# Performance work log

Measured on AMD Instinct MI355X. Metric: run time of the kernel, lower is better.

Reference implementation:

```python
import jax, jax.numpy as jnp
import numpy as np

EPS = 1e-5  # BatchNorm eps
TOPK = 256  # SoftThresholdingOperation topk


def conv1x1(x, W, b):
    # x: [B,C,H,W], W: [O,C], b: [O]
    return jnp.einsum('bchw,oc->bohw', x, W) + b[None, :, None, None]


def bn_relu(x, gamma, beta, mean, var):
    # inference-mode BatchNorm2d followed by ReLU
    inv = gamma / jnp.sqrt(var + EPS)
    return jax.nn.relu(x * inv[None, :, None, None] + (beta - mean * inv)[None, :, None, None])


def topk_sparsemax(x, k):
    # HSPA SoftThresholdingOperation: sparsemax restricted to top-k entries of last axis.
    k = min(k, x.shape[-1])
    vals = jax.lax.top_k(x, k)[0]                       # sorted descending, [..., k]
    cssv = jnp.cumsum(vals, axis=-1) - 1.0              # cumulative sum minus 1
    r = jnp.arange(1, k + 1, dtype=x.dtype)
    support = vals * r > cssv                           # support indicator
    k_sup = jnp.sum(support, axis=-1, keepdims=True)    # support size, int
    tau = jnp.take_along_axis(cssv, k_sup - 1, axis=-1) / k_sup.astype(x.dtype)
    return jnp.clip(x - tau, 0.0)                       # sparse attention weights


def setup_inputs() -> dict:
    key = jax.random.key(0)
    ks = jax.random.split(key, 10)
    B, C = 128, 256
    s = 1.0 / np.sqrt(C)
    return {
        'zf': jax.random.normal(ks[0], (B, C, 13, 13), jnp.float32),
        'xf': jax.random.normal(ks[1], (B, C, 25, 25), jnp.float32),
        'Wq': jax.random.normal(ks[2], (C, C), jnp.float32) * s,
        'bq': jnp.zeros((C,), jnp.float32),
        'Ws': jax.random.normal(ks[3], (C, C), jnp.float32) * s,
        'bs': jnp.zeros((C,), jnp.float32),
        'Wg': jax.random.normal(ks[4], (C, C), jnp.float32) * s,
        'bg': jnp.zeros((C,), jnp.float32),
        'g_gamma': jnp.ones((C,), jnp.float32),
        'g_beta': jnp.zeros((C,), jnp.float32),
        'g_mean': jnp.zeros((C,), jnp.float32),
        'g_var': jnp.ones((C,), jnp.float32),
        'Wf': jax.random.normal(ks[5], (C, 2 * C), jnp.float32) * (1.0 / np.sqrt(2 * C)),
        'bf': jnp.zeros((C,), jnp.float32),
        'f_gamma': jnp.ones((C,), jnp.float32),
        'f_beta': jnp.zeros((C,), jnp.float32),
        'f_mean': jnp.zeros((C,), jnp.float32),
        'f_var': jnp.ones((C,), jnp.float32),
    }


def reference(zf, xf, Wq, bq, Ws, bs, Wg, bg, g_gamma, g_beta, g_mean, g_var,
              Wf, bf, f_gamma, f_beta, f_mean, f_var):
    B, C, Hx, Wx = xf.shape
    _, _, Hz, Wz = zf.shape
    xf_trans = conv1x1(xf, Wq, bq)                      # query
    zf_trans = conv1x1(zf, Ws, bs)                      # support
    xf_g = bn_relu(conv1x1(xf, Wg, bg), g_gamma, g_beta, g_mean, g_var)
    zf_g = bn_relu(conv1x1(zf, Wg, bg), g_gamma, g_beta, g_mean, g_var)

    Nx, Nz = Hx * Wx, Hz * Wz
    zf_trans_p = zf_trans.reshape(B, C, Nz)             # [B,C,Nz]
    zf_g_p = zf_g.reshape(B, C, Nz)                     # [B,C,Nz]
    xf_trans_p = xf_trans.reshape(B, C, Nx)             # [B,C,Nx]

    similar = jnp.einsum('bcn,bcm->bnm', xf_trans_p, zf_trans_p)  # [B,Nx,Nz]
    score = topk_sparsemax(similar, TOPK)                          # sparse attn
    embedding = jnp.einsum('bnm,bcm->bcn', score, zf_g_p)          # [B,C,Nx]
    embedding = embedding.reshape(B, C, Hx, Wx)

    cat = jnp.concatenate([embedding, xf_g], axis=1)    # [B,2C,Hx,Wx]
    out = bn_relu(conv1x1(cat, Wf, bf), f_gamma, f_beta, f_mean, f_var)
    return out
```

## Files before the change

### kernel.cpp

```cpp
#include <hip/hip_runtime.h>
#include <math.h>

#define EPS 1e-5f

constexpr int Bb  = 128;
constexpr int C   = 256;
constexpr int Nz  = 169;
constexpr int Nx  = 625;
constexpr int NzP = 192;

typedef __bf16 bf16x8 __attribute__((ext_vector_type(8)));
typedef float  f32x4  __attribute__((ext_vector_type(4)));

__device__ __forceinline__ unsigned short f2bf(float f) {
    union { float f; unsigned u; } x; x.f = f;
    unsigned r = x.u + 0x7FFFu + ((x.u >> 16) & 1u);
    return (unsigned short)(r >> 16);
}
__device__ __forceinline__ float bf2f(unsigned short h) {
    union { unsigned u; float f; } x; x.u = ((unsigned)h) << 16;
    return x.f;
}

__global__ __launch_bounds__(256)
void prep_all(const float* __restrict__ zf,
              const float* __restrict__ Wq, const float* __restrict__ bq,
              const float* __restrict__ Ws, const float* __restrict__ bs,
              const float* __restrict__ Wg, const float* __restrict__ Wf,
              unsigned short* __restrict__ Wg_bf, unsigned short* __restrict__ Wf_bf,
              float* __restrict__ wv, float* __restrict__ wu, float* __restrict__ c0,
              unsigned short* __restrict__ Mhi, unsigned short* __restrict__ Mlo,
              float* __restrict__ U,
              unsigned short* __restrict__ zfT_hi, unsigned short* __restrict__ zfT_lo)
{
    __shared__ float T[64][65];
    const int bx = blockIdx.x, tid = threadIdx.x;

    if (bx < 512) {
        int i = bx * 256 + tid;
        if (i < C * C) Wg_bf[i] = f2bf(Wg[i]);
        if (i < C * 2 * C) Wf_bf[i] = f2bf(Wf[i]);
        return;
    }
    if (bx == 512) {
        float a = 0.f, b = 0.f;
        for (int o = 0; o < C; ++o) {
            a += Wq[o * C + tid] * bs[o];
            b += Ws[o * C + tid] * bq[o];
        }
        wv[tid] = a;
        wu[tid] = b;
        if (tid == 0) {
            float c = 0.f;
            for (int o = 0; o < C; ++o) c += bq[o] * bs[o];
            c0[0] = c;
        }
        return;
    }
    if (bx < 529) {
        const int t  = bx - 513;
        const int j0 = (t & 3) * 64, i0 = (t >> 2) * 64;
        const int tx = tid & 15, ty = tid >> 4;
        float (*Qs)[65] = (float(*)[65])&T[0][0];
        float (*Ss)[65] = (float(*)[65])&T[16][0];
        float acc[4][4] = {};

        for (int kc = 0; kc < C; kc += 16) {
            #pragma unroll
            for (int i = 0; i < 4; ++i) {
                int e = tid + 256 * i;
                int k = e >> 6, col = e & 63;
                Qs[k][col] = Wq[(size_t)(kc + k) * C + i0 + col];
                Ss[k][col] = Ws[(size_t)(kc + k) * C + j0 + col];
            }
            __syncthreads();
            #pragma unroll
            for (int k = 0; k < 16; ++k) {
                float a[4], bv[4];
                #pragma unroll
                for (int i = 0; i < 4; ++i) a[i] = Qs[k][ty * 4 + i];
                #pragma unroll
                for (int j = 0; j < 4; ++j) bv[j] = Ss[k][tx * 4 + j];
                #pragma unroll
                for (int i = 0; i < 4; ++i)
                    #pragma unroll
                    for (int j = 0; j < 4; ++j)
                        acc[i][j] = fmaf(a[i], bv[j], acc[i][j]);
            }
            __syncthreads();
        }
        #pragma unroll
        for (int i = 0; i < 4; ++i)
            #pragma unroll
            for (int j = 0; j < 4; ++j) {
                float v = acc[i][j];
                unsigned short h = f2bf(v);
                size_t idx = (size_t)(i0 + ty * 4 + i) * C + j0 + tx * 4 + j;
                Mhi[idx] = h;
                Mlo[idx] = f2bf(v - bf2f(h));
            }
        return;
    }
    if (bx < 657) {
        const int b = bx - 529, m = tid;
        if (m >= NzP) return;
        float s = 0.f;
        if (m < Nz) {
            const float* zb = zf + (size_t)b * C * Nz + m;
            float s0 = 0.f, s1 = 0.f, s2 = 0.f, s3 = 0.f;
            for (int c = 0; c < C; c += 4) {
                s0 += wu[c]     * zb[(size_t)c * Nz];
                s1 += wu[c + 1] * zb[(size_t)(c + 1) * Nz];
                s2 += wu[c + 2] * zb[(size_t)(c + 2) * Nz];
                s3 += wu[c + 3] * zb[(size_t)(c + 3) * Nz];
            }
            s = (s0 + s1) + (s2 + s3) + c0[0];
        }
        U[(size_t)b * NzP + m] = s;
        return;
    }
    {
        const int t  = bx - 657;
        const int n0 = (t % 3) * 64;
        const int c0v = ((t / 3) & 3) * 64;
        const int b  = t / 12;
        const float* Xb = zf + ((size_t)b * C + c0v) * Nz;
        #pragma unroll
        for (int i = 0; i < 16; ++i) {
            int e = tid + 256 * i;
            int c = e >> 6, n = e & 63;
            T[c][n] = (n0 + n < Nz) ? Xb[(size_t)c * Nz + n0 + n] : 0.f;
        }
        __syncthreads();
        #pragma unroll
        for (int i = 0; i < 16; ++i) {
            int e = tid + 256 * i;
            int n = e >> 6, c = e & 63;
            if (n0 + n < Nz) {
                float v = T[c][n];
                unsigned short h = f2bf(v);
                size_t idx = ((size_t)b * Nz + n0 + n) * C + c0v + c;
                zfT_hi[idx] = h;
                zfT_lo[idx] = f2bf(v - bf2f(h));
            }
        }
    }
}

__global__ __launch_bounds__(256)
void z_gemm(const unsigned short* __restrict__ Mhi,
            const unsigned short* __restrict__ Mlo,
            const unsigned short* __restrict__ Wg,
            const unsigned short* __restrict__ Bhi,
            const unsigned short* __restrict__ Blo,
            const float* __restrict__ wv,
            const float* __restrict__ bg, const float* __restrict__ g_gamma,
            const float* __restrict__ g_beta, const float* __restrict__ g_mean,
            const float* __restrict__ g_var,
            unsigned short* __restrict__ Yqh, unsigned short* __restrict__ Yql,
            unsigned short* __restrict__ Yg)
{
    __shared__ unsigned short Ah[64][40], Al[64][40], Ag[64][40];
    __shared__ unsigned short Bh[64][40], Bl[64][40];

    const int b   = blockIdx.z;
    const int n0  = blockIdx.x * 64;
    const int o0  = blockIdx.y * 64;
    const int tid = threadIdx.x;
    const int lane = tid & 63, wid = tid >> 6;
    const int wr = wid >> 1, wc = wid & 1;

    const unsigned short* Bhb = Bhi + (size_t)b * Nz * C;
    const unsigned short* Blb = Blo + (size_t)b * Nz * C;

    f32x4 accq[2][2], accg[2][2];
    #pragma unroll
    for (int i = 0; i < 2; ++i)
        #pragma unroll
        for (int j = 0; j < 2; ++j)
            #pragma unroll
            for (int e = 0; e < 4; ++e) { accq[i][j][e] = 0.f; accg[i][j][e] = 0.f; }

    const int srow = tid >> 2, sseg = tid & 3;
    const int lr = lane & 15, lk = (lane >> 4) * 8;

    for (int kc = 0; kc < C; kc += 32) {
        const int gk = kc + sseg * 8;
        *(int4*)&Ah[srow][sseg * 8] = *(const int4*)&Mhi[(size_t)(o0 + srow) * C + gk];
        *(int4*)&Al[srow][sseg * 8] = *(const int4*)&Mlo[(size_t)(o0 + srow) * C + gk];
        *(int4*)&Ag[srow][sseg * 8] = *(const int4*)&Wg[(size_t)(o0 + srow) * C + gk];

        const int gn = n0 + srow;
        int4 bv = make_int4(0, 0, 0, 0), blv = make_int4(0, 0, 0, 0);
        if (gn < Nz) {
            bv  = *(const int4*)&Bhb[(size_t)gn * C + gk];
            blv = *(const int4*)&Blb[(size_t)gn * C + gk];
        }
        *(int4*)&Bh[srow][sseg * 8] = bv;
        *(int4*)&Bl[srow][sseg * 8] = blv;
        __syncthreads();

        bf16x8 ah[2], al[2], ag[2], bh[2], bl[2];
        #pragma unroll
        for (int i = 0; i < 2; ++i) {
            ah[i] = *(const bf16x8*)&Ah[wr * 32 + i * 16 + lr][lk];
            al[i] = *(const bf16x8*)&Al[wr * 32 + i * 16 + lr][lk];
            ag[i] = *(const bf16x8*)&Ag[wr * 32 + i * 16 + lr][lk];
            bh[i] = *(const bf16x8*)&Bh[wc * 32 + i * 16 + lr][lk];
            bl[i] = *(const bf16x8*)&Bl[wc * 32 + i * 16 + lr][lk];
        }
        #pragma unroll
        for (int i = 0; i < 2; ++i)
            #pragma unroll
            for (int j = 0; j < 2; ++j) {
                accq[i][j] = __builtin_amdgcn_mfma_f32_16x16x32_bf16(al[i], bh[j], accq[i][j], 0, 0, 0);
                accq[i][j] = __builtin_amdgcn_mfma_f32_16x16x32_bf16(ah[i], bl[j], accq[i][j], 0, 0, 0);
                accq[i][j] = __builtin_amdgcn_mfma_f32_16x16x32_bf16(ah[i], bh[j], accq[i][j], 0, 0, 0);
                accg[i][j] = __builtin_amdgcn_mfma_f32_16x16x32_bf16(ag[i], bh[j], accg[i][j], 0, 0, 0);
            }
        __syncthreads();
    }

    const int lg = lane >> 4;
    #pragma unroll
    for (int i = 0; i < 2; ++i) {
        const int ob = o0 + wr * 32 + i * 16 + lg * 4;
        float bi[4], inv[4], sh[4], bgi[4];
        #pragma unroll
        for (int r = 0; r < 4; ++r) {
            int o = ob + r;
            bi[r] = wv[o];
            float iv = g_gamma[o] * rsqrtf(g_var[o] + EPS);
            inv[r] = iv; sh[r] = g_beta[o] - g_mean[o] * iv; bgi[r] = bg[o];
        }
        #pragma unroll
        for (int j = 0; j < 2; ++j) {
            const int gn = n0 + wc * 32 + j * 16 + lr;
            uint2 ph = make_uint2(0, 0), pl = make_uint2(0, 0), pg = make_uint2(0, 0);
            if (gn < Nz) {
                unsigned short h[4], l[4], g[4];
                #pragma unroll
                for (int r = 0; r < 4; ++r) {
                    float v = accq[i][j][r] + bi[r];
                    h[r] = f2bf(v);
                    l[r] = f2bf(v - bf2f(h[r]));
                    g[r] = f2bf(fmaxf(fmaf(accg[i][j][r] + bgi[r], inv[r], sh[r]), 0.f));
                }
                ph.x = (unsigned)h[0] | ((unsigned)h[1] << 16);
                ph.y = (unsigned)h[2] | ((unsigned)h[3] << 16);
                pl.x = (unsigned)l[0] | ((unsigned)l[1] << 16);
                pl.y = (unsigned)l[2] | ((unsigned)l[3] << 16);
                pg.x = (unsigned)g[0] | ((unsigned)g[1] << 16);
                pg.y = (unsigned)g[2] | ((unsigned)g[3] << 16);
            }
            size_t idx = ((size_t)b * NzP + gn) * C + ob;
            *(uint2*)&Yqh[idx] = ph;
            *(uint2*)&Yql[idx] = pl;
            *(uint2*)&Yg[idx]  = pg;
        }
    }
}

__global__ __launch_bounds__(256)
void zg2_gemm(const unsigned short* __restrict__ A, int aLd,
              const unsigned short* __restrict__ B1,
              unsigned short* __restrict__ Y, int N, int Nout, int K, int O)
{
    __shared__ unsigned short As[64][40];
    __shared__ unsigned short Bs[64][40];

    const int b   = blockIdx.z;
    const int n0  = blockIdx.x * 64;
    const int o0  = blockIdx.y * 64;
    const int tid = threadIdx.x;
    const int lane = tid & 63, wid = tid >> 6;
    const int wr = wid >> 1, wc = wid & 1;

    const unsigned short* B1b = B1 + (size_t)b * N * K;

    f32x4 acc[2][2];
    #pragma unroll
    for (int i = 0; i < 2; ++i)
        #pragma unroll
        for (int j = 0; j < 2; ++j)
            #pragma unroll
            for (int e = 0; e < 4; ++e) acc[i][j][e] = 0.f;

    const int srow = tid >> 2, sseg = tid & 3;
    const int lr = lane & 15, lk = (lane >> 4) * 8;

    for (int kc = 0; kc < K; kc += 32) {
        const int gk = kc + sseg * 8;
        *(int4*)&As[srow][sseg * 8] = *(const int4*)&A[(size_t)(o0 + srow) * aLd + gk];

        const int gn = n0 + srow;
        int4 bv = make_int4(0, 0, 0, 0);
        if (gn < N) bv = *(const int4*)&B1b[(size_t)gn * K + gk];
        *(int4*)&Bs[srow][sseg * 8] = bv;
        __syncthreads();

        bf16x8 a0 = *(const bf16x8*)&As[wr * 32 +      lr][lk];
        bf16x8 a1 = *(const bf16x8*)&As[wr * 32 + 16 + lr][lk];
        bf16x8 b0 = *(const bf16x8*)&Bs[wc * 32 +      lr][lk];
        bf16x8 b1 = *(const bf16x8*)&Bs[wc * 32 + 16 + lr][lk];

        acc[0][0] = __builtin_amdgcn_mfma_f32_16x16x32_bf16(a0, b0, acc[0][0], 0, 0, 0);
        acc[0][1] = __builtin_amdgcn_mfma_f32_16x16x32_bf16(a0, b1, acc[0][1], 0, 0, 0);
        acc[1][0] = __builtin_amdgcn_mfma_f32_16x16x32_bf16(a1, b0, acc[1][0], 0, 0, 0);
        acc[1][1] = __builtin_amdgcn_mfma_f32_16x16x32_bf16(a1, b1, acc[1][1], 0, 0, 0);
        __syncthreads();
    }

    const int lg = lane >> 4;
    #pragma unroll
    for (int i = 0; i < 2; ++i) {
        const int ob = o0 + wr * 32 + i * 16 + lg * 4;
        #pragma unroll
        for (int j = 0; j < 2; ++j) {
            const int gn = n0 + wc * 32 + j * 16 + lr;
            if (gn < Nout) {
                #pragma unroll
                for (int r = 0; r < 4; ++r)
                    Y[((size_t)b * O + ob + r) * Nout + gn] =
                        (gn < N) ? f2bf(acc[i][j][r]) : (unsigned short)0;
            }
        }
    }
}

#define XGIDX(n, o) ((((n) << 8) + (o)) ^ (((n) & 7) << 3))

__global__ __launch_bounds__(256)
void mega_x(const float* __restrict__ Xf,
            const unsigned short* __restrict__ Zqh,
            const unsigned short* __restrict__ Zql,
            const unsigned short* __restrict__ Wg,
            const unsigned short* __restrict__ Zg2,
            const unsigned short* __restrict__ Wf2,
            const float* __restrict__ U,
            const float* __restrict__ bg, const float* __restrict__ g_gamma,
            const float* __restrict__ g_beta, const float* __restrict__ g_mean,
            const float* __restrict__ g_var,
            const float* __restrict__ bf, const float* __restrict__ f_gamma,
            const float* __restrict__ f_beta, const float* __restrict__ f_mean,
            const float* __restrict__ f_var,
            float* __restrict__ out)
{
    __shared__ __attribute__((aligned(16))) char pool[69632];
    __shared__ float Us[192];

    unsigned short* XFfull = (unsigned short*)(pool);
    unsigned short* XG     = (unsigned short*)(pool);
    unsigned short* Bzh    = (unsigned short*)(pool + 33792);
    unsigned short* Bzl    = (unsigned short*)(pool + 49152);
    unsigned short* Ssc    = (unsigned short*)(pool + 33792);
    unsigned short* XFl    = (unsigned short*)(pool + 64512);

    const int g0  = blockIdx.z * gridDim.x + blockIdx.x;
    const int rid = (g0 & 7) * 160 + (g0 >> 3);
    const int b   = rid / 10;
    const int n0  = (rid % 10) * 64;

    const int tid = threadIdx.x;
    const int lane = tid & 63, w = tid >> 6;
    const int lr = lane & 15, lg = lane >> 4, lk = lg * 8;
    const int brow = tid >> 2, bseg = tid & 3;

    const unsigned short* Zqhb = Zqh + (size_t)b * NzP * C;
    const unsigned short* Zqlb = Zql + (size_t)b * NzP * C;
    const unsigned short* Zg2b = Zg2 + (size_t)b * C * NzP;

    if (tid < 192) Us[tid] = U[(size_t)b * NzP + tid];

    const int gnA = min(n0 + brow, Nx - 1);

    {
        f32x4 sacc[12];
        #pragma unroll
        for (int j = 0; j < 12; ++j)
            #pragma unroll
            for (int e = 0; e < 4; ++e) sacc[j][e] = 0.f;

        for (int kc = 0; kc < C; kc += 32) {
            {
                const float* src = Xf + ((size_t)b * C + kc + bseg * 8) * Nx + gnA;
                unsigned short h[8], l[8];
                #pragma unroll
                for (int e = 0; e < 8; ++e) {
                    float v = src[(size_t)e * Nx];
                    h[e] = f2bf(v);
                    l[e] = f2bf(v - bf2f(h[e]));
                }
                uint4 ph, pl;
                ph.x = (unsigned)h[0] | ((unsigned)h[1] << 16);
                ph.y = (unsigned)h[2] | ((unsigned)h[3] << 16);
                ph.z = (unsigned)h[4] | ((unsigned)h[5] << 16);
                ph.w = (unsigned)h[6] | ((unsigned)h[7] << 16);
                pl.x = (unsigned)l[0] | ((unsigned)l[1] << 16);
                pl.y = (unsigned)l[2] | ((unsigned)l[3] << 16);
                pl.z = (unsigned)l[4] | ((unsigned)l[5] << 16);
                pl.w = (unsigned)l[6] | ((unsigned)l[7] << 16);
                *(uint4*)&XFfull[brow * 264 + kc + bseg * 8] = ph;
                *(uint4*)&XFl[brow * 40 + bseg * 8] = pl;
            }
            #pragma unroll
            for (int i = 0; i < 3; ++i) {
                const int slot = tid + 256 * i;
                const int r = slot >> 2, s = slot & 3;
                const int gk = kc + s * 8;
                *(int4*)&Bzh[r * 40 + s * 8] = *(const int4*)&Zqhb[(size_t)r * C + gk];
                *(int4*)&Bzl[r * 40 + s * 8] = *(const int4*)&Zqlb[(size_t)r * C + gk];
            }
            __syncthreads();

            bf16x8 a0h = *(const bf16x8*)&XFfull[(w * 16 + lr) * 264 + kc + lk];
            bf16x8 a0l = *(const bf16x8*)&XFl[(w * 16 + lr) * 40 + lk];
            #pragma unroll
            for (int j = 0; j < 12; ++j) {
                bf16x8 bh = *(const bf16x8*)&Bzh[(j * 16 + lr) * 40 + lk];
                bf16x8 bl = *(const bf16x8*)&Bzl[(j * 16 + lr) * 40 + lk];
                sacc[j] = __builtin_amdgcn_mfma_f32_16x16x32_bf16(a0l, bh, sacc[j], 0, 0, 0);
                sacc[j] = __builtin_amdgcn_mfma_f32_16x16x32_bf16(a0h, bl, sacc[j], 0, 0, 0);
                sacc[j] = __builtin_amdgcn_mfma_f32_16x16x32_bf16(a0h, bh, sacc[j], 0, 0, 0);
            }
            __syncthreads();
        }

        #pragma unroll
        for (int j = 0; j < 12; ++j) {
            const int m = j * 16 + lr;
            const float uv = Us[m];
            const bool bad = (m >= Nz);
            #pragma unroll
            for (int q = 0; q < 4; ++q)
                sacc[j][q] = bad ? -1e30f : (sacc[j][q] + uv);
        }

        f32x4 mx = sacc[0];
        #pragma unroll
        for (int j = 1; j < 12; ++j)
            #pragma unroll
            for (int q = 0; q < 4; ++q) mx[q] = fmaxf(mx[q], sacc[j][q]);
        #pragma unroll
        for (int off = 1; off < 16; off <<= 1)
            #pragma unroll
            for (int q = 0; q < 4; ++q) mx[q] = fmaxf(mx[q], __shfl_xor(mx[q], off));

        f32x4 tau;
        #pragma unroll
        for (int q = 0; q < 4; ++q) tau[q] = mx[q] - 1.0f;

        for (int it = 0; it < 16; ++it) {
            f32x4 s, cnt;
            #pragma unroll
            for (int q = 0; q < 4; ++q) { s[q] = 0.f; cnt[q] = 0.f; }
            #pragma unroll
            for (int j = 0; j < 12; ++j)
                #pragma unroll
                for (int q = 0; q < 4; ++q)
                    if (sacc[j][q] > tau[q]) { s[q] += sacc[j][q]; cnt[q] += 1.f; }
            #pragma unroll
            for (int off = 1; off < 16; off <<= 1)
                #pragma unroll
                for (int q = 0; q < 4; ++q) {
                    s[q]   += __shfl_xor(s[q], off);
                    cnt[q] += __shfl_xor(cnt[q], off);
                }
            bool adv = false;
            #pragma unroll
            for (int q = 0; q < 4; ++q) {
                float nt = (s[q] - 1.0f) / cnt[q];
                if (nt > tau[q]) { tau[q] = nt; adv = true; }
            }
            if (!__any(adv ? 1 : 0)) break;
        }

        #pragma unroll
        for (int q = 0; q < 4; ++q) {
            const int n = w * 16 + 4 * lg + q;
            #pragma unroll
            for (int j = 0; j < 12; ++j) {
                const int m = j * 16 + lr;
                float sv = (m < Nz) ? fmaxf(sacc[j][q] - tau[q], 0.f) : 0.f;
                Ssc[n * 200 + m] = f2bf(sv);
            }
        }
    }

    f32x4 acc[4][4];
    #pragma unroll
    for (int i = 0; i < 4; ++i)
        #pragma unroll
        for (int j = 0; j < 4; ++j)
            #pragma unroll
            for (int e = 0; e < 4; ++e) acc[i][j][e] = 0.f;

    #pragma unroll
    for (int c = 0; c < 8; ++c) {
        const int kc = c * 32;
        bf16x8 a[4], bfr[4];
        #pragma unroll
        for (int i = 0; i < 4; ++i)
            a[i] = *(const bf16x8*)&Wg[(size_t)(w * 64 + i * 16 + lr) * C + kc + lk];
        #pragma unroll
        for (int j = 0; j < 4; ++j)
            bfr[j] = *(const bf16x8*)&XFfull[(j * 16 + lr) * 264 + kc + lk];
        #pragma unroll
        for (int i = 0; i < 4; ++i)
            #pragma unroll
            for (int j = 0; j < 4; ++j)
                acc[i][j] = __builtin_amdgcn_mfma_f32_16x16x32_bf16(a[i], bfr[j], acc[i][j], 0, 0, 0);
    }
    __syncthreads();

    #pragma unroll
    for (int i = 0; i < 4; ++i) {
        const int ob = w * 64 + i * 16 + lg * 4;
        float inv[4], sh[4], bi[4];
        #pragma unroll
        for (int r = 0; r < 4; ++r) {
            int o = ob + r;
            float iv = g_gamma[o] * rsqrtf(g_var[o] + EPS);
            inv[r] = iv; sh[r] = g_beta[o] - g_mean[o] * iv; bi[r] = bg[o];
        }
        #pragma unroll
        for (int j = 0; j < 4; ++j) {
            const int n = j * 16 + lr;
            unsigned short h[4];
            #pragma unroll
            for (int r = 0; r < 4; ++r)
                h[r] = f2bf(fmaxf(fmaf(acc[i][j][r] + bi[r], inv[r], sh[r]), 0.f));
            uint2 pk;
            pk.x = (unsigned)h[0] | ((unsigned)h[1] << 16);
            pk.y = (unsigned)h[2] | ((unsigned)h[3] << 16);
            *(uint2*)&XG[XGIDX(n, ob)] = pk;
        }
    }
    #pragma unroll
    for (int i = 0; i < 4; ++i)
        #pragma unroll
        for (int j = 0; j < 4; ++j)
            #pragma unroll
            for (int e = 0; e < 4; ++e) acc[i][j][e] = 0.f;
    __syncthreads();

    #pragma unroll
    for (int c = 0; c < 6; ++c) {
        const int kc = c * 32;
        bf16x8 a[4], bfr[4];
        #pragma unroll
        for (int i = 0; i < 4; ++i)
            a[i] = *(const bf16x8*)&Zg2b[(size_t)(w * 64 + i * 16 + lr) * NzP + kc + lk];
        #pragma unroll
        for (int j = 0; j < 4; ++j)
            bfr[j] = *(const bf16x8*)&Ssc[(j * 16 + lr) * 200 + kc + lk];
        #pragma unroll
        for (int i = 0; i < 4; ++i)
            #pragma unroll
            for (int j = 0; j < 4; ++j)
                acc[i][j] = __builtin_amdgcn_mfma_f32_16x16x32_bf16(a[i], bfr[j], acc[i][j], 0, 0, 0);
    }

    #pragma unroll
    for (int c = 0; c < 8; ++c) {
        const int kc = c * 32;
        bf16x8 a[4], bfr[4];
        #pragma unroll
        for (int i = 0; i < 4; ++i)
            a[i] = *(const bf16x8*)&Wf2[(size_t)(w * 64 + i * 16 + lr) * 512 + kc + lk];
        #pragma unroll
        for (int j = 0; j < 4; ++j)
            bfr[j] = *(const bf16x8*)&XG[XGIDX(j * 16 + lr, kc + lk)];
        #pragma unroll
        for (int i = 0; i < 4; ++i)
            #pragma unroll
            for (int j = 0; j < 4; ++j)
                acc[i][j] = __builtin_amdgcn_mfma_f32_16x16x32_bf16(a[i], bfr[j], acc[i][j], 0, 0, 0);
    }

    #pragma unroll
    for (int i = 0; i < 4; ++i) {
        const int ob = w * 64 + i * 16 + lg * 4;
        float inv[4], sh[4], bi[4];
        #pragma unroll
        for (int r = 0; r < 4; ++r) {
            int o = ob + r;
            float iv = f_gamma[o] * rsqrtf(f_var[o] + EPS);
            inv[r] = iv; sh[r] = f_beta[o] - f_mean[o] * iv; bi[r] = bf[o];
        }
        #pragma unroll
        for (int j = 0; j < 4; ++j) {
            const int gn = n0 + j * 16 + lr;
            if (gn < Nx) {
                #pragma unroll
                for (int r = 0; r < 4; ++r) {
                    float v = fmaxf(fmaf(acc[i][j][r] + bi[r], inv[r], sh[r]), 0.f);
                    out[((size_t)b * C + ob + r) * Nx + gn] = v;
                }
            }
        }
    }
}

extern "C" void kernel_launch(void* const* d_in, const int* in_sizes, int n_in,
                              void* d_out, int out_size, void* d_ws, size_t ws_size,
                              hipStream_t stream)
{
    const float* zf      = (const float*)d_in[0];
    const float* xf      = (const float*)d_in[1];
    const float* Wq      = (const float*)d_in[2];
    const float* bq      = (const float*)d_in[3];
    const float* Ws_     = (const float*)d_in[4];
    const float* bs      = (const float*)d_in[5];
    const float* Wg      = (const float*)d_in[6];
    const float* bg      = (const float*)d_in[7];
    const float* g_gamma = (const float*)d_in[8];
    const float* g_beta  = (const float*)d_in[9];
    const float* g_mean  = (const float*)d_in[10];
    const float* g_var   = (const float*)d_in[11];
    const float* Wf      = (const float*)d_in[12];
    const float* bf_     = (const float*)d_in[13];
    const float* f_gamma = (const float*)d_in[14];
    const float* f_beta  = (const float*)d_in[15];
    const float* f_mean  = (const float*)d_in[16];
    const float* f_var   = (const float*)d_in[17];
    float* out = (float*)d_out;

    typedef unsigned short u16;
    char* ws = (char*)d_ws;
    u16*   zfT_hi = (u16*)(ws);
    u16*   zfT_lo = (u16*)(ws +  11075584);
    u16*   zqT_hi = (u16*)(ws +  22151168);
    u16*   zqT_lo = (u16*)(ws +  34734080);
    u16*   zf_gT  = (u16*)(ws +  47316992);
    u16*   zg2    = (u16*)(ws +  59899904);
    float* U      = (float*)(ws +  72482816);
    u16*   Mhi    = (u16*)(ws +  72581120);
    u16*   Mlo    = (u16*)(ws +  72712192);
    u16*   Wg_bf  = (u16*)(ws +  72843264);
    u16*   Wf_bf  = (u16*)(ws +  72974336);
    float* wv     = (float*)(ws +  73236480);
    float* wu     = (float*)(ws +  73237504);
    float* c0     = (float*)(ws +  73238528);

    dim3 blk(256);
    const int gx_x = (Nx + 63) / 64;
    const int gx_z = NzP / 64;

    prep_all<<<dim3(2193), blk, 0, stream>>>(
        zf, Wq, bq, Ws_, bs, Wg, Wf,
        Wg_bf, Wf_bf, wv, wu, c0, Mhi, Mlo, U, zfT_hi, zfT_lo);

    z_gemm<<<dim3(gx_z, C / 64, Bb), blk, 0, stream>>>(
        Mhi, Mlo, Wg_bf, zfT_hi, zfT_lo, wv,
        bg, g_gamma, g_beta, g_mean, g_var,
        zqT_hi, zqT_lo, zf_gT);

    zg2_gemm<<<dim3(gx_z, C / 64, Bb), blk, 0, stream>>>(
        Wf_bf, 2 * C, zf_gT, zg2, NzP, NzP, C, C);

    mega_x<<<dim3(gx_x, 1, Bb), blk, 0, stream>>>(
        xf, zqT_hi, zqT_lo, Wg_bf, zg2, Wf_bf + C, U,
        bg, g_gamma, g_beta, g_mean, g_var,
        bf_, f_gamma, f_beta, f_mean, f_var, out);
}
```

Baseline: 199.0 us.

## Fuse z-side transpose, U, query/gate GEMMs and Wf projection into one kernel

Replaces the zf transpose/split, U reduction, z_gemm and zg2_gemm stages with a single z_full kernel. Each block loads a 64-column slice of zf once into LDS as bf16 hi/lo, computes U, the split-precision query projection, and the gated BN-ReLU features, then applies the Wf projection from LDS. This removes two kernel launches and the global round-trips of zfT and zf_gT. In exchange, each block covers all 256 output channels, giving only 384 blocks with large LDS use. Weight fragments are now read straight from global memory instead of being staged in shared memory.

```diff
diff --git a/kernel.cpp b/kernel.cpp
--- a/kernel.cpp
+++ b/kernel.cpp
@@ -23,17 +23,14 @@
 }
 
 __global__ __launch_bounds__(256)
-void prep_all(const float* __restrict__ zf,
-              const float* __restrict__ Wq, const float* __restrict__ bq,
+void prep_all(const float* __restrict__ Wq, const float* __restrict__ bq,
               const float* __restrict__ Ws, const float* __restrict__ bs,
               const float* __restrict__ Wg, const float* __restrict__ Wf,
               unsigned short* __restrict__ Wg_bf, unsigned short* __restrict__ Wf_bf,
               float* __restrict__ wv, float* __restrict__ wu, float* __restrict__ c0,
-              unsigned short* __restrict__ Mhi, unsigned short* __restrict__ Mlo,
-              float* __restrict__ U,
-              unsigned short* __restrict__ zfT_hi, unsigned short* __restrict__ zfT_lo)
+              unsigned short* __restrict__ Mhi, unsigned short* __restrict__ Mlo)
 {
-    __shared__ float T[64][65];
+    __shared__ float T[32][65];
     const int bx = blockIdx.x, tid = threadIdx.x;
 
     if (bx < 512) {
@@ -57,7 +54,7 @@
         }
         return;
     }
-    if (bx < 529) {
+    {
         const int t  = bx - 513;
         const int j0 = (t & 3) * 64, i0 = (t >> 2) * 64;
         const int tx = tid & 15, ty = tid >> 4;
@@ -99,231 +96,227 @@
                 Mhi[idx] = h;
                 Mlo[idx] = f2bf(v - bf2f(h));
             }
-        return;
-    }
-    if (bx < 657) {
-        const int b = bx - 529, m = tid;
-        if (m >= NzP) return;
-        float s = 0.f;
-        if (m < Nz) {
-            const float* zb = zf + (size_t)b * C * Nz + m;
-            float s0 = 0.f, s1 = 0.f, s2 = 0.f, s3 = 0.f;
-            for (int c = 0; c < C; c += 4) {
-                s0 += wu[c]     * zb[(size_t)c * Nz];
-                s1 += wu[c + 1] * zb[(size_t)(c + 1) * Nz];
-                s2 += wu[c + 2] * zb[(size_t)(c + 2) * Nz];
-                s3 += wu[c + 3] * zb[(size_t)(c + 3) * Nz];
-            }
-            s = (s0 + s1) + (s2 + s3) + c0[0];
-        }
-        U[(size_t)b * NzP + m] = s;
-        return;
-    }
-    {
-        const int t  = bx - 657;
-        const int n0 = (t % 3) * 64;
-        const int c0v = ((t / 3) & 3) * 64;
-        const int b  = t / 12;
-        const float* Xb = zf + ((size_t)b * C + c0v) * Nz;
-        #pragma unroll
-        for (int i = 0; i < 16; ++i) {
-            int e = tid + 256 * i;
-            int c = e >> 6, n = e & 63;
-            T[c][n] = (n0 + n < Nz) ? Xb[(size_t)c * Nz + n0 + n] : 0.f;
-        }
-        __syncthreads();
-        #pragma unroll
-        for (int i = 0; i < 16; ++i) {
-            int e = tid + 256 * i;
-            int n = e >> 6, c = e & 63;
-            if (n0 + n < Nz) {
-                float v = T[c][n];
-                unsigned short h = f2bf(v);
-                size_t idx = ((size_t)b * Nz + n0 + n) * C + c0v + c;
-                zfT_hi[idx] = h;
-                zfT_lo[idx] = f2bf(v - bf2f(h));
-            }
-        }
     }
 }
 
 __global__ __launch_bounds__(256)
-void z_gemm(const unsigned short* __restrict__ Mhi,
+void z_full(const float* __restrict__ zf,
+            const unsigned short* __restrict__ Mhi,
             const unsigned short* __restrict__ Mlo,
             const unsigned short* __restrict__ Wg,
-            const unsigned short* __restrict__ Bhi,
-            const unsigned short* __restrict__ Blo,
-            const float* __restrict__ wv,
+            const unsigned short* __restrict__ Wf1,
+            const float* __restrict__ wv, const float* __restrict__ wu,
+            const float* __restrict__ c0,
             const float* __restrict__ bg, const float* __restrict__ g_gamma,
             const float* __restrict__ g_beta, const float* __restrict__ g_mean,
             const float* __restrict__ g_var,
             unsigned short* __restrict__ Yqh, unsigned short* __restrict__ Yql,
-            unsigned short* __restrict__ Yg)
+            unsigned short* __restrict__ Zg2out, float* __restrict__ U)
 {
-    __shared__ unsigned short Ah[64][40], Al[64][40], Ag[64][40];
-    __shared__ unsigned short Bh[64][40], Bl[64][40];
-
-    const int b   = blockIdx.z;
-    const int n0  = blockIdx.x * 64;
-    const int o0  = blockIdx.y * 64;
+    __shared__ __attribute__((aligned(16))) char pool[67584];
+    __shared__ float UP[64][5];
+
+    unsigned short* Zh = (unsigned short*)(pool);
+    unsigned short* Zl = (unsigned short*)(pool + 33792);
+    unsigned short* ZG = (unsigned short*)(pool + 33792);
+
+    const int b  = blockIdx.z;
+    const int n0 = blockIdx.x * 64;
+
     const int tid = threadIdx.x;
-    const int lane = tid & 63, wid = tid >> 6;
-    const int wr = wid >> 1, wc = wid & 1;
-
-    const unsigned short* Bhb = Bhi + (size_t)b * Nz * C;
-    const unsigned short* Blb = Blo + (size_t)b * Nz * C;
-
-    f32x4 accq[2][2], accg[2][2];
-    #pragma unroll
-    for (int i = 0; i < 2; ++i)
-        #pragma unroll
-        for (int j = 0; j < 2; ++j)
-            #pragma unroll
-            for (int e = 0; e < 4; ++e) { accq[i][j][e] = 0.f; accg[i][j][e] = 0.f; }
-
-    const int srow = tid >> 2, sseg = tid & 3;
-    const int lr = lane & 15, lk = (lane >> 4) * 8;
-
-    for (int kc = 0; kc < C; kc += 32) {
-        const int gk = kc + sseg * 8;
-        *(int4*)&Ah[srow][sseg * 8] = *(const int4*)&Mhi[(size_t)(o0 + srow) * C + gk];
-        *(int4*)&Al[srow][sseg * 8] = *(const int4*)&Mlo[(size_t)(o0 + srow) * C + gk];
-        *(int4*)&Ag[srow][sseg * 8] = *(const int4*)&Wg[(size_t)(o0 + srow) * C + gk];
-
-        const int gn = n0 + srow;
-        int4 bv = make_int4(0, 0, 0, 0), blv = make_int4(0, 0, 0, 0);
-        if (gn < Nz) {
-            bv  = *(const int4*)&Bhb[(size_t)gn * C + gk];
-            blv = *(const int4*)&Blb[(size_t)gn * C + gk];
-        }
-        *(int4*)&Bh[srow][sseg * 8] = bv;
-        *(int4*)&Bl[srow][sseg * 8] = blv;
-        __syncthreads();
-
-        bf16x8 ah[2], al[2], ag[2], bh[2], bl[2];
-        #pragma unroll
-        for (int i = 0; i < 2; ++i) {
-            ah[i] = *(const bf16x8*)&Ah[wr * 32 + i * 16 + lr][lk];
-            al[i] = *(const bf16x8*)&Al[wr * 32 + i * 16 + lr][lk];
-            ag[i] = *(const bf16x8*)&Ag[wr * 32 + i * 16 + lr][lk];
-            bh[i] = *(const bf16x8*)&Bh[wc * 32 + i * 16 + lr][lk];
-            bl[i] = *(const bf16x8*)&Bl[wc * 32 + i * 16 + lr][lk];
-        }
-        #pragma unroll
-        for (int i = 0; i < 2; ++i)
-            #pragma unroll
-            for (int j = 0; j < 2; ++j) {
-                accq[i][j] = __builtin_amdgcn_mfma_f32_16x16x32_bf16(al[i], bh[j], accq[i][j], 0, 0, 0);
-                accq[i][j] = __builtin_amdgcn_mfma_f32_16x16x32_bf16(ah[i], bl[j], accq[i][j], 0, 0, 0);
-                accq[i][j] = __builtin_amdgcn_mfma_f32_16x16x32_bf16(ah[i], bh[j], accq[i][j], 0, 0, 0);
-                accg[i][j] = __builtin_amdgcn_mfma_f32_16x16x32_bf16(ag[i], bh[j], accg[i][j], 0, 0, 0);
-            }
-        __syncthreads();
-    }
-
-    const int lg = lane >> 4;
-    #pragma unroll
-    for (int i = 0; i < 2; ++i) {
-        const int ob = o0 + wr * 32 + i * 16 + lg * 4;
-        float bi[4], inv[4], sh[4], bgi[4];
+    const int lane = tid & 63, w = tid >> 6;
+    const int lr = lane & 15, lg = lane >> 4, lk = lg * 8;
+    const int brow = tid >> 2, bseg = tid & 3;
+
+    const int gnA = min(n0 + brow, Nz - 1);
+
+    #pragma unroll
+    for (int c = 0; c < 8; ++c) {
+        const int kc = c * 32;
+        const float* src = zf + ((size_t)b * C + kc + bseg * 8) * Nz + gnA;
+        unsigned short h[8], l[8];
+        #pragma unroll
+        for (int e = 0; e < 8; ++e) {
+            float v = src[(size_t)e * Nz];
+            h[e] = f2bf(v);
+            l[e] = f2bf(v - bf2f(h[e]));
+        }
+        uint4 ph, pl;
+        ph.x = (unsigned)h[0] | ((unsigned)h[1] << 16);
+        ph.y = (unsigned)h[2] | ((unsigned)h[3] << 16);
+        ph.z = (unsigned)h[4] | ((unsigned)h[5] << 16);
+        ph.w = (unsigned)h[6] | ((unsigned)h[7] << 16);
+        pl.x = (unsigned)l[0] | ((unsigned)l[1] << 16);
+        pl.y = (unsigned)l[2] | ((unsigned)l[3] << 16);
+        pl.z = (unsigned)l[4] | ((unsigned)l[5] << 16);
+        pl.w = (unsigned)l[6] | ((unsigned)l[7] << 16);
+        *(uint4*)&Zh[brow * 264 + kc + bseg * 8] = ph;
+        *(uint4*)&Zl[brow * 264 + kc + bseg * 8] = pl;
+    }
+    __syncthreads();
+
+    {
+        const int r = tid & 63, q = tid >> 6;
+        float s = 0.f;
+        for (int k = q * 64; k < q * 64 + 64; ++k)
+            s += wu[k] * (bf2f(Zh[r * 264 + k]) + bf2f(Zl[r * 264 + k]));
+        UP[r][q] = s;
+    }
+    __syncthreads();
+    if (tid < 64) {
+        const int gn = n0 + tid;
+        float val = 0.f;
+        if (gn < Nz)
+            val = UP[tid][0] + UP[tid][1] + UP[tid][2] + UP[tid][3] + c0[0];
+        U[(size_t)b * NzP + gn] = val;
+    }
+
+    {
+        f32x4 accq[4][4];
+        #pragma unroll
+        for (int i = 0; i < 4; ++i)
+            #pragma unroll
+            for (int j = 0; j < 4; ++j)
+                #pragma unroll
+                for (int e = 0; e < 4; ++e) accq[i][j][e] = 0.f;
+
+        #pragma unroll
+        for (int c = 0; c < 8; ++c) {
+            const int kc = c * 32;
+            bf16x8 ah[4], al[4], bh[4], bl[4];
+            #pragma unroll
+            for (int i = 0; i < 4; ++i) {
+                ah[i] = *(const bf16x8*)&Mhi[(size_t)(w * 64 + i * 16 + lr) * C + kc + lk];
+                al[i] = *(const bf16x8*)&Mlo[(size_t)(w * 64 + i * 16 + lr) * C + kc + lk];
+            }
+            #pragma unroll
+            for (int j = 0; j < 4; ++j) {
+                bh[j] = *(const bf16x8*)&Zh[(j * 16 + lr) * 264 + kc + lk];
+                bl[j] = *(const bf16x8*)&Zl[(j * 16 + lr) * 264 + kc + lk];
+            }
+            #pragma unroll
+            for (int i = 0; i < 4; ++i)
+                #pragma unroll
+                for (int j = 0; j < 4; ++j) {
+                    accq[i][j] = __builtin_amdgcn_mfma_f32_16x16x32_bf16(al[i], bh[j], accq[i][j], 0, 0, 0);
+                    accq[i][j] = __builtin_amdgcn_mfma_f32_16x16x32_bf16(ah[i], bl[j], accq[i][j], 0, 0, 0);
+                    accq[i][j] = __builtin_amdgcn_mfma_f32_16x16x32_bf16(ah[i], bh[j], accq[i][j], 0, 0, 0);
+                }
+        }
+
+        #pragma unroll
+        for (int i = 0; i < 4; ++i) {
+            const int ob = w * 64 + i * 16 + lg * 4;
+            float bi[4];
+            #pragma unroll
+            for (int r = 0; r < 4; ++r) bi[r] = wv[ob + r];
+            #pragma unroll
+            for (int j = 0; j < 4; ++j) {
+                const int gn = n0 + j * 16 + lr;
+                uint2 ph = make_uint2(0, 0), pl = make_uint2(0, 0);
+                if (gn < Nz) {
+                    unsigned short h[4], l[4];
+                    #pragma unroll
+                    for (int r = 0; r < 4; ++r) {
+                        float v = accq[i][j][r] + bi[r];
+                        h[r] = f2bf(v);
+                        l[r] = f2bf(v - bf2f(h[r]));
+                    }
+                    ph.x = (unsigned)h[0] | ((unsigned)h[1] << 16);
+                    ph.y = (unsigned)h[2] | ((unsigned)h[3] << 16);
+                    pl.x = (unsigned)l[0] | ((unsigned)l[1] << 16);
+                    pl.y = (unsigned)l[2] | ((unsigned)l[3] << 16);
+                }
+                size_t idx = ((size_t)b * NzP + gn) * C + ob;
+                *(uint2*)&Yqh[idx] = ph;
+                *(uint2*)&Yql[idx] = pl;
+            }
+        }
+    }
+
+    f32x4 acc[4][4];
+    #pragma unroll
+    for (int i = 0; i < 4; ++i)
+        #pragma unroll
+        for (int j = 0; j < 4; ++j)
+            #pragma unroll
+            for (int e = 0; e < 4; ++e) acc[i][j][e] = 0.f;
+
+    #pragma unroll
+    for (int c = 0; c < 8; ++c) {
+        const int kc = c * 32;
+        bf16x8 a[4], bfr[4];
+        #pragma unroll
+        for (int i = 0; i < 4; ++i)
+            a[i] = *(const bf16x8*)&Wg[(size_t)(w * 64 + i * 16 + lr) * C + kc + lk];
+        #pragma unroll
+        for (int j = 0; j < 4; ++j)
+            bfr[j] = *(const bf16x8*)&Zh[(j * 16 + lr) * 264 + kc + lk];
+        #pragma unroll
+        for (int i = 0; i < 4; ++i)
+            #pragma unroll
+            for (int j = 0; j < 4; ++j)
+                acc[i][j] = __builtin_amdgcn_mfma_f32_16x16x32_bf16(a[i], bfr[j], acc[i][j], 0, 0, 0);
+    }
+    __syncthreads();
+
+    #pragma unroll
+    for (int i = 0; i < 4; ++i) {
+        const int ob = w * 64 + i * 16 + lg * 4;
+        float inv[4], sh[4], bi[4];
         #pragma unroll
         for (int r = 0; r < 4; ++r) {
             int o = ob + r;
-            bi[r] = wv[o];
             float iv = g_gamma[o] * rsqrtf(g_var[o] + EPS);
-            inv[r] = iv; sh[r] = g_beta[o] - g_mean[o] * iv; bgi[r] = bg[o];
-        }
-        #pragma unroll
-        for (int j = 0; j < 2; ++j) {
-            const int gn = n0 + wc * 32 + j * 16 + lr;
-            uint2 ph = make_uint2(0, 0), pl = make_uint2(0, 0), pg = make_uint2(0, 0);
-            if (gn < Nz) {
-                unsigned short h[4], l[4], g[4];
-                #pragma unroll
-                for (int r = 0; r < 4; ++r) {
-                    float v = accq[i][j][r] + bi[r];
-                    h[r] = f2bf(v);
-                    l[r] = f2bf(v - bf2f(h[r]));
-                    g[r] = f2bf(fmaxf(fmaf(accg[i][j][r] + bgi[r], inv[r], sh[r]), 0.f));
-                }
-                ph.x = (unsigned)h[0] | ((unsigned)h[1] << 16);
-                ph.y = (unsigned)h[2] | ((unsigned)h[3] << 16);
-                pl.x = (unsigned)l[0] | ((unsigned)l[1] << 16);
-                pl.y = (unsigned)l[2] | ((unsigned)l[3] << 16);
-                pg.x = (unsigned)g[0] | ((unsigned)g[1] << 16);
-                pg.y = (unsigned)g[2] | ((unsigned)g[3] << 16);
-            }
-            size_t idx = ((size_t)b * NzP + gn) * C + ob;
-            *(uint2*)&Yqh[idx] = ph;
-            *(uint2*)&Yql[idx] = pl;
-            *(uint2*)&Yg[idx]  = pg;
-        }
-    }
-}
-
-__global__ __launch_bounds__(256)
-void zg2_gemm(const unsigned short* __restrict__ A, int aLd,
-              const unsigned short* __restrict__ B1,
-              unsigned short* __restrict__ Y, int N, int Nout, int K, int O)
-{
-    __shared__ unsigned short As[64][40];
-    __shared__ unsigned short Bs[64][40];
-
-    const int b   = blockIdx.z;
-    const int n0  = blockIdx.x * 64;
-    const int o0  = blockIdx.y * 64;
-    const int tid = threadIdx.x;
-    const int lane = tid & 63, wid = tid >> 6;
-    const int wr = wid >> 1, wc = wid & 1;
-
-    const unsigned short* B1b = B1 + (size_t)b * N * K;
-
-    f32x4 acc[2][2];
-    #pragma unroll
-    for (int i = 0; i < 2; ++i)
-        #pragma unroll
-        for (int j = 0; j < 2; ++j)
+            inv[r] = iv; sh[r] = g_beta[o] - g_mean[o] * iv; bi[r] = bg[o];
+        }
+        #pragma unroll
+        for (int j = 0; j < 4; ++j) {
+            const int n = j * 16 + lr;
+            unsigned short h[4];
+            #pragma unroll
+            for (int r = 0; r < 4; ++r)
+                h[r] = f2bf(fmaxf(fmaf(acc[i][j][r] + bi[r], inv[r], sh[r]), 0.f));
+            uint2 pk;
+            pk.x = (unsigned)h[0] | ((unsigned)h[1] << 16);
+            pk.y = (unsigned)h[2] | ((unsigned)h[3] << 16);
+            *(uint2*)&ZG[n * 264 + ob] = pk;
+        }
+    }
+    #pragma unroll
+    for (int i = 0; i < 4; ++i)
+        #pragma unroll
+        for (int j = 0; j < 4; ++j)
             #pragma unroll
             for (int e = 0; e < 4; ++e) acc[i][j][e] = 0.f;
-
-    const int srow = tid >> 2, sseg = tid & 3;
-    const int lr = lane & 15, lk = (lane >> 4) * 8;
-
-    for (int kc = 0; kc < K; kc += 32) {
-        const int gk = kc + sseg * 8;
-        *(int4*)&As[srow][sseg * 8] = *(const int4*)&A[(size_t)(o0 + srow) * aLd + gk];
-
-        const int gn = n0 + srow;
-        int4 bv = make_int4(0, 0, 0, 0);
-        if (gn < N) bv = *(const int4*)&B1b[(size_t)gn * K + gk];
-        *(int4*)&Bs[srow][sseg * 8] = bv;
-        __syncthreads();
-
-        bf16x8 a0 = *(const bf16x8*)&As[wr * 32 +      lr][lk];
-        bf16x8 a1 = *(const bf16x8*)&As[wr * 32 + 16 + lr][lk];
-        bf16x8 b0 = *(const bf16x8*)&Bs[wc * 32 +      lr][lk];
-        bf16x8 b1 = *(const bf16x8*)&Bs[wc * 32 + 16 + lr][lk];
-
-        acc[0][0] = __builtin_amdgcn_mfma_f32_16x16x32_bf16(a0, b0, acc[0][0], 0, 0, 0);
-        acc[0][1] = __builtin_amdgcn_mfma_f32_16x16x32_bf16(a0, b1, acc[0][1], 0, 0, 0);
-        acc[1][0] = __builtin_amdgcn_mfma_f32_16x16x32_bf16(a1, b0, acc[1][0], 0, 0, 0);
-        acc[1][1] = __builtin_amdgcn_mfma_f32_16x16x32_bf16(a1, b1, acc[1][1], 0, 0, 0);
-        __syncthreads();
-    }
-
-    const int lg = lane >> 4;
-    #pragma unroll
-    for (int i = 0; i < 2; ++i) {
-        const int ob = o0 + wr * 32 + i * 16 + lg * 4;
-        #pragma unroll
-        for (int j = 0; j < 2; ++j) {
-            const int gn = n0 + wc * 32 + j * 16 + lr;
-            if (gn < Nout) {
-                #pragma unroll
-                for (int r = 0; r < 4; ++r)
-                    Y[((size_t)b * O + ob + r) * Nout + gn] =
-                        (gn < N) ? f2bf(acc[i][j][r]) : (unsigned short)0;
-            }
+    __syncthreads();
+
+    #pragma unroll
+    for (int c = 0; c < 8; ++c) {
+        const int kc = c * 32;
+        bf16x8 a[4], bfr[4];
+        #pragma unroll
+        for (int i = 0; i < 4; ++i)
+            a[i] = *(const bf16x8*)&Wf1[(size_t)(w * 64 + i * 16 + lr) * 512 + kc + lk];
+        #pragma unroll
+        for (int j = 0; j < 4; ++j)
+            bfr[j] = *(const bf16x8*)&ZG[(j * 16 + lr) * 264 + kc + lk];
+        #pragma unroll
+        for (int i = 0; i < 4; ++i)
+            #pragma unroll
+            for (int j = 0; j < 4; ++j)
+                acc[i][j] = __builtin_amdgcn_mfma_f32_16x16x32_bf16(a[i], bfr[j], acc[i][j], 0, 0, 0);
+    }
+
+    #pragma unroll
+    for (int i = 0; i < 4; ++i) {
+        const int ob = w * 64 + i * 16 + lg * 4;
+        #pragma unroll
+        for (int j = 0; j < 4; ++j) {
+            const int gm = n0 + j * 16 + lr;
+            #pragma unroll
+            for (int r = 0; r < 4; ++r)
+                Zg2out[((size_t)b * C + ob + r) * NzP + gm] = f2bf(acc[i][j][r]);
         }
     }
 }
@@ -628,36 +621,30 @@
 
     typedef unsigned short u16;
     char* ws = (char*)d_ws;
-    u16*   zfT_hi = (u16*)(ws);
-    u16*   zfT_lo = (u16*)(ws +  11075584);
-    u16*   zqT_hi = (u16*)(ws +  22151168);
-    u16*   zqT_lo = (u16*)(ws +  34734080);
-    u16*   zf_gT  = (u16*)(ws +  47316992);
-    u16*   zg2    = (u16*)(ws +  59899904);
-    float* U      = (float*)(ws +  72482816);
-    u16*   Mhi    = (u16*)(ws +  72581120);
-    u16*   Mlo    = (u16*)(ws +  72712192);
-    u16*   Wg_bf  = (u16*)(ws +  72843264);
-    u16*   Wf_bf  = (u16*)(ws +  72974336);
-    float* wv     = (float*)(ws +  73236480);
-    float* wu     = (float*)(ws +  73237504);
-    float* c0     = (float*)(ws +  73238528);
+    u16*   zqT_hi = (u16*)(ws);
+    u16*   zqT_lo = (u16*)(ws +  12582912);
+    u16*   zg2    = (u16*)(ws +  25165824);
+    float* U      = (float*)(ws +  37748736);
+    u16*   Mhi    = (u16*)(ws +  37847040);
+    u16*   Mlo    = (u16*)(ws +  37978112);
+    u16*   Wg_bf  = (u16*)(ws +  38109184);
+    u16*   Wf_bf  = (u16*)(ws +  38240256);
+    float* wv     = (float*)(ws +  38502400);
+    float* wu     = (float*)(ws +  38503424);
+    float* c0     = (float*)(ws +  38504448);
 
     dim3 blk(256);
     const int gx_x = (Nx + 63) / 64;
     const int gx_z = NzP / 64;
 
-    prep_all<<<dim3(2193), blk, 0, stream>>>(
-        zf, Wq, bq, Ws_, bs, Wg, Wf,
-        Wg_bf, Wf_bf, wv, wu, c0, Mhi, Mlo, U, zfT_hi, zfT_lo);
-
-    z_gemm<<<dim3(gx_z, C / 64, Bb), blk, 0, stream>>>(
-        Mhi, Mlo, Wg_bf, zfT_hi, zfT_lo, wv,
+    prep_all<<<dim3(529), blk, 0, stream>>>(
+        Wq, bq, Ws_, bs, Wg, Wf,
+        Wg_bf, Wf_bf, wv, wu, c0, Mhi, Mlo);
+
+    z_full<<<dim3(gx_z, 1, Bb), blk, 0, stream>>>(
+        zf, Mhi, Mlo, Wg_bf, Wf_bf, wv, wu, c0,
         bg, g_gamma, g_beta, g_mean, g_var,
-        zqT_hi, zqT_lo, zf_gT);
-
-    zg2_gemm<<<dim3(gx_z, C / 64, Bb), blk, 0, stream>>>(
-        Wf_bf, 2 * C, zf_gT, zg2, NzP, NzP, C, C);
+        zqT_hi, zqT_lo, zg2, U);
 
     mega_x<<<dim3(gx_x, 1, Bb), blk, 0, stream>>>(
         xf, zqT_hi, zqT_lo, Wg_bf, zg2, Wf_bf + C, U,
```

Result: faster. 189.2 us (-4.9%).
